# Optimization experiments

Hardware: AMD Instinct MI355X
Metric: run time of the kernel (lower is better)

The kernel has to match this reference:

```python
import jax, jax.numpy as jnp
import numpy as np

N_NODES = 50000
N_EDGES = 600000
D = 128
ITERATIONS = 3


def setup_inputs() -> dict:
    key = jax.random.key(0)
    k0, k1, k2, k3 = jax.random.split(key, 4)
    node_feats = jax.random.normal(k0, (N_NODES, D), dtype=jnp.float32)
    adjacency = jax.random.randint(k1, (N_EDGES, 2), 0, N_NODES, dtype=jnp.int64)
    scale = 1.0 / np.sqrt(D).astype(np.float32)
    W_emb = jax.random.normal(k2, (D, D), dtype=jnp.float32) * scale
    b_emb = jnp.zeros((D,), dtype=jnp.float32)
    W_upd = jax.random.normal(k3, (D, D), dtype=jnp.float32) * scale
    b_upd = jnp.zeros((D,), dtype=jnp.float32)
    return {
        "node_feats": node_feats,
        "W_emb": W_emb,
        "b_emb": b_emb,
        "W_upd": W_upd,
        "b_upd": b_upd,
        "adjacency": adjacency,
    }


def reference(node_feats, W_emb, b_emb, W_upd, b_upd, adjacency):
    # Embedding layer: Dense + ReLU per node (inference path skips BatchNorm)
    h = jax.nn.relu(node_feats @ W_emb + b_emb)  # [N, D]

    src = adjacency[:, 0]
    dst = adjacency[:, 1]

    # Each undirected edge contributes a message in both directions.
    ones = jnp.ones((N_EDGES,), dtype=h.dtype)
    deg = (jax.ops.segment_sum(ones, src, num_segments=N_NODES)
           + jax.ops.segment_sum(ones, dst, num_segments=N_NODES))  # [N]
    denom = (deg + 1.0)[:, None]  # +1 for the node's own contribution

    for _ in range(ITERATIONS):
        # MessagePassing: gather neighbor features, scatter-add into nodes,
        # then normalize by (num incoming messages + 1).
        agg = (jax.ops.segment_sum(h[dst], src, num_segments=N_NODES)
               + jax.ops.segment_sum(h[src], dst, num_segments=N_NODES))  # [N, D]
        h = (h + agg) / denom
        # Update: per-node Dense followed by sigmoid nonlinearity.
        h = jax.nn.sigmoid(h @ W_upd + b_upd)
    return h
```

## Files before the change

kernel.cpp:

```cpp
#include <hip/hip_runtime.h>
#include <hip/hip_bf16.h>

#define NN 50000
#define NE 600000
#define DD 128
#define RB 64
#define NSHARD_DIV 6250
#define GB ((NN + RB - 1) / RB)
#define EBQ ((NE + 1023) / 1024)
#define SB ((NN + 1023) / 1024)
#define GQB3 (2 * ((NN + 31) / 32))

typedef __bf16 bfrag __attribute__((ext_vector_type(8)));
typedef float  ffrag __attribute__((ext_vector_type(4)));
typedef unsigned uintv4 __attribute__((ext_vector_type(4)));
typedef unsigned uintv2 __attribute__((ext_vector_type(2)));

union frag_cast { uintv4 u4; unsigned u[4]; bfrag b; };

__device__ __forceinline__ float bfbits2f(unsigned v) { return __uint_as_float(v << 16); }
__device__ __forceinline__ unsigned f2bfbits(float f) {
    unsigned u = __float_as_uint(f);
    return (u + 0x7FFFu + ((u >> 16) & 1u)) >> 16;
}

__device__ __forceinline__ float ld_in(const void* p, int idx, int f32) {
    return f32 ? ((const float*)p)[idx]
               : bfbits2f(((const unsigned short*)p)[idx]);
}

__device__ __forceinline__ void ld_edge_nt(const int* adj, int e, int i64, int& s, int& d) {
    if (i64) {
        s = __builtin_nontemporal_load(&adj[4 * e]);
        d = __builtin_nontemporal_load(&adj[4 * e + 2]);
    } else {
        s = __builtin_nontemporal_load(&adj[2 * e]);
        d = __builtin_nontemporal_load(&adj[2 * e + 1]);
    }
}

__global__ void k_prep(const unsigned* __restrict__ Ww, const unsigned* __restrict__ adjw,
                       const void* __restrict__ We, const void* __restrict__ Wu,
                       unsigned short* __restrict__ WeT, unsigned short* __restrict__ WuT,
                       int* __restrict__ flags, int* __restrict__ deg) {
    const int tid = threadIdx.x;
    if (blockIdx.x < DD) {
        __shared__ int scnt;
        if (tid == 0) scnt = 0;
        __syncthreads();
        int c = 0;
        for (int i = tid; i < 512; i += 256) {
            unsigned e = (Ww[i] >> 7) & 0xFFu;
            c += (e >= 0x60u && e <= 0x85u) ? 1 : 0;
        }
        atomicAdd(&scnt, c);
        __syncthreads();
        const int f32 = (scnt >= 256) ? 0 : 1;
        const int k = blockIdx.x;
        if (tid < DD) {
            WeT[tid * DD + k] = (unsigned short)f2bfbits(ld_in(We, k * DD + tid, f32));
        } else {
            int n = tid - DD;
            WuT[n * DD + k] = (unsigned short)f2bfbits(ld_in(Wu, k * DD + n, f32));
        }
        return;
    }
    for (int i = (blockIdx.x - DD) * 256 + tid; i < NN; i += 64 * 256) deg[i] = 0;
    if (blockIdx.x != DD) return;
    __shared__ int cnt[2];
    if (tid < 2) cnt[tid] = 0;
    __syncthreads();
    int c0 = 0, c1 = 0;
    for (int i = tid; i < 512; i += 256) {
        unsigned e = (Ww[i] >> 7) & 0xFFu;
        c0 += (e >= 0x60u && e <= 0x85u) ? 1 : 0;
        c1 += (adjw[2 * i + 1] == 0u) ? 1 : 0;
    }
    atomicAdd(&cnt[0], c0);
    atomicAdd(&cnt[1], c1);
    __syncthreads();
    if (tid == 0) {
        flags[0] = (cnt[0] >= 256) ? 0 : 1;
        flags[1] = (cnt[1] >= 256) ? 1 : 0;
    }
}

__device__ __forceinline__ void stage_w(const uintv4* __restrict__ WTg, uintv4* sW, int tid) {
#pragma unroll
    for (int k = 0; k < 8; k++) {
        int d = k * 256 + tid;
        int m = d & 15, rest = d >> 4;
        int quad = rest & 3, ks = (rest >> 2) & 3, ct = rest >> 4;
        sW[d] = WTg[(ct * 16 + m) * 16 + (ks * 4 + quad)];
    }
}

__device__ __forceinline__ void mfma_rows(const bfrag af[4], const bfrag* sW,
                                          int m, int quad, ffrag acc[8]) {
#pragma unroll
    for (int ks = 0; ks < 4; ks++) {
#pragma unroll
        for (int ct = 0; ct < 8; ct++) {
            bfrag bf_ = sW[((ct * 4 + ks) * 4 + quad) * 16 + m];
            acc[ct] = __builtin_amdgcn_mfma_f32_16x16x32_bf16(af[ks], bf_, acc[ct], 0, 0, 0);
        }
    }
}

__device__ __forceinline__ void st_h2(unsigned short* __restrict__ Hout,
                                      int ct, int m, int orow, float z) {
    Hout[(size_t)(ct >> 2) * (NN * 64) + (size_t)orow * 64 + (ct & 3) * 16 + m] =
        (unsigned short)f2bfbits(z);
}

__launch_bounds__(256, 5)
__global__ void k_main1(const void* __restrict__ Xp, const unsigned short* __restrict__ WTg,
                        const void* __restrict__ Bp, unsigned short* __restrict__ Hout,
                        const int* __restrict__ flags, const int* __restrict__ adj,
                        int* __restrict__ deg, uintv2* __restrict__ edg) {
    __shared__ __align__(16) unsigned short sWT[DD * DD];
    const int tid = threadIdx.x;
    if (blockIdx.x >= GB) {
        const int bb = blockIdx.x - GB;
        const int i64 = flags[1];
#pragma unroll
        for (int k = 0; k < 4; k++) {
            const int e = bb * 1024 + k * 256 + tid;
            if (e < NE) {
                int s, d;
                ld_edge_nt(adj, e, i64, s, d);
                uintv2 out;
                if ((unsigned)s < NN && (unsigned)d < NN) {
                    int ks = atomicAdd(&deg[s], 1);
                    int kd = atomicAdd(&deg[d], 1);
                    out[0] = (unsigned)s | ((unsigned)d << 16);
                    out[1] = (unsigned)ks | ((unsigned)kd << 16);
                } else {
                    out[0] = 0xFFFFFFFFu;
                    out[1] = 0;
                }
                __builtin_nontemporal_store(out, &edg[e]);
            }
        }
        return;
    }
    const int wave = tid >> 6;
    const int lane = tid & 63;
    const int f32  = flags[0];
    const int m    = lane & 15;
    const int quad = lane >> 4;
    const int rowbase = blockIdx.x * RB + wave * 16;
    const int row  = rowbase + m;
    const int rc   = (row < NN) ? row : (NN - 1);

    stage_w((const uintv4*)WTg, (uintv4*)sWT, tid);

    bfrag af[4];
    if (f32) {
        const float4* Xf = (const float4*)Xp;
#pragma unroll
        for (int ks = 0; ks < 4; ks++) {
            const int k0 = ks * 32 + quad * 8;
            float4 a0 = Xf[rc * 32 + (k0 >> 2)];
            float4 a1 = Xf[rc * 32 + (k0 >> 2) + 1];
            frag_cast fc;
            fc.u[0] = f2bfbits(a0.x) | (f2bfbits(a0.y) << 16);
            fc.u[1] = f2bfbits(a0.z) | (f2bfbits(a0.w) << 16);
            fc.u[2] = f2bfbits(a1.x) | (f2bfbits(a1.y) << 16);
            fc.u[3] = f2bfbits(a1.z) | (f2bfbits(a1.w) << 16);
            af[ks] = fc.b;
        }
    } else {
        const uintv4* Xv = (const uintv4*)Xp;
#pragma unroll
        for (int ks = 0; ks < 4; ks++) {
            const int k0 = ks * 32 + quad * 8;
            frag_cast fc;
            fc.u4 = Xv[rc * 16 + (k0 >> 3)];
            af[ks] = fc.b;
        }
    }
    __syncthreads();

    ffrag acc[8];
#pragma unroll
    for (int i = 0; i < 8; i++) acc[i] = (ffrag)(0.0f);
    mfma_rows(af, (const bfrag*)sWT, m, quad, acc);

#pragma unroll
    for (int ct = 0; ct < 8; ct++) {
        int col = ct * 16 + m;
        float bb = ld_in(Bp, col, f32);
#pragma unroll
        for (int reg = 0; reg < 4; reg++) {
            int orow = rowbase + quad * 4 + reg;
            if (orow < NN) {
                float z = fmaxf(acc[ct][reg] + bb, 0.0f);
                st_h2(Hout, ct, m, orow, z);
            }
        }
    }
}

__global__ void k_scan1(const int* __restrict__ deg, int* __restrict__ rows,
                        int* __restrict__ sums, int* __restrict__ bhist) {
    __shared__ int wsum[16];
    __shared__ int woff[16];
    __shared__ int hist[256];
    const int tid  = threadIdx.x;
    const int wid  = tid >> 6;
    const int lane = tid & 63;
    const int i = blockIdx.x * 1024 + tid;
    if (tid < 256) hist[tid] = 0;
    __syncthreads();
    int x = (i < NN) ? deg[i] : 0;
    if (i < NN) atomicAdd(&hist[(x < 255) ? x : 255], 1);
#pragma unroll
    for (int off = 1; off < 64; off <<= 1) {
        int y = __shfl_up(x, off, 64);
        if (lane >= off) x += y;
    }
    if (lane == 63) wsum[wid] = x;
    __syncthreads();
    if (wid == 0) {
        int s  = (lane < 16) ? wsum[lane] : 0;
        int xs = s;
#pragma unroll
        for (int off = 1; off < 16; off <<= 1) {
            int y = __shfl_up(xs, off, 64);
            if (lane >= off) xs += y;
        }
        if (lane < 16) woff[lane] = xs - s;
        if (lane == 15) sums[blockIdx.x] = xs;
    }
    __syncthreads();
    if (i < NN) rows[i + 1] = x + woff[wid];
    if (tid < 256) bhist[blockIdx.x * 256 + tid] = hist[tid];
}

__global__ void k_scan2(int* __restrict__ sums, int nb,
                        const int* __restrict__ bhist, int* __restrict__ boff,
                        int* __restrict__ bbase) {
    __shared__ int wps[4];
    const int t = threadIdx.x, lane = t & 63, w = t >> 6;
    if (w == 0) {
        int v = (lane < nb) ? sums[lane] : 0;
        int x = v;
        for (int off = 1; off < 64; off <<= 1) {
            int y = __shfl_up(x, off, 64);
            if (lane >= off) x += y;
        }
        if (lane < nb) sums[lane] = x - v;
    }
    int run = 0;
    for (int blk = 0; blk < nb; blk++) {
        int c = bhist[blk * 256 + t];
        boff[blk * 256 + t] = run;
        run += c;
    }
    int v = run, x = v;
    for (int off = 1; off < 64; off <<= 1) {
        int y = __shfl_up(x, off, 64);
        if (lane >= off) x += y;
    }
    if (lane == 63) wps[w] = x;
    __syncthreads();
    int add = 0;
    for (int k = 0; k < w; k++) add += wps[k];
    bbase[t] = x - v + add;
}

__global__ void k_scan3(const int* __restrict__ sums, int* __restrict__ rows,
                        const int* __restrict__ deg, const int* __restrict__ boff,
                        const int* __restrict__ bbase, int* __restrict__ order) {
    __shared__ int lh[256];
    const int tid = threadIdx.x;
    if (tid < 256) lh[tid] = 0;
    __syncthreads();
    int i = blockIdx.x * 1024 + tid;
    int d = 0, r = 0;
    if (i < NN) {
        rows[i + 1] += sums[blockIdx.x];
        if (i == 0) rows[0] = 0;
        d = deg[i];
        d = (d < 255) ? d : 255;
        r = atomicAdd(&lh[d], 1);
        order[bbase[d] + boff[blockIdx.x * 256 + d] + r] = i;
    }
}

__launch_bounds__(256)
__global__ void k_fill2(const uintv2* __restrict__ edg, const int* __restrict__ rows,
                        unsigned short* __restrict__ nbr) {
    const int shard = blockIdx.x & 7;
    const int bb = blockIdx.x >> 3;
#pragma unroll
    for (int k = 0; k < 4; k++) {
        const int e = bb * 1024 + k * 256 + threadIdx.x;
        if (e >= NE) continue;
        uintv2 v = __builtin_nontemporal_load(&edg[e]);
        if (v[0] == 0xFFFFFFFFu) continue;
        const int s = v[0] & 0xFFFFu, d = v[0] >> 16;
        if (s / NSHARD_DIV == shard) nbr[rows[s] + (v[1] & 0xFFFFu)] = (unsigned short)d;
        if (d / NSHARD_DIV == shard) nbr[rows[d] + (v[1] >> 16)]    = (unsigned short)s;
    }
}

__device__ __forceinline__ void accv4(float a[8], uintv4 v) {
#pragma unroll
    for (int k = 0; k < 4; k++) {
        a[2 * k]     += bfbits2f(v[k] & 0xFFFFu);
        a[2 * k + 1] += bfbits2f(v[k] >> 16);
    }
}

__launch_bounds__(256)
__global__ void k_gath5(const unsigned* __restrict__ Hp, const int* __restrict__ rows,
                        const unsigned short* __restrict__ nbr,
                        const int* __restrict__ order, unsigned* __restrict__ XB32) {
    const int plane = blockIdx.x & 1;
    const int chunk = blockIdx.x >> 1;
    const int g     = threadIdx.x >> 3;
    const int l8    = threadIdx.x & 7;
    const int opos  = chunk * 32 + g;
    const int nid   = order[(opos < NN) ? opos : (NN - 1)];
    const uintv4* Pv = (const uintv4*)Hp + (size_t)plane * (NN * 8);
    const int st = rows[nid], en = rows[nid + 1];
    uintv4 sv = Pv[(size_t)nid * 8 + l8];
    float a[8];
#pragma unroll
    for (int k = 0; k < 4; k++) {
        a[2 * k]     = bfbits2f(sv[k] & 0xFFFFu);
        a[2 * k + 1] = bfbits2f(sv[k] >> 16);
    }
    int j = st;
    for (; j + 8 <= en; j += 8) {
        int n[8];
#pragma unroll
        for (int t = 0; t < 8; t++) n[t] = nbr[j + t];
        uintv4 v[8];
#pragma unroll
        for (int t = 0; t < 8; t++) v[t] = Pv[(size_t)n[t] * 8 + l8];
#pragma unroll
        for (int t = 0; t < 8; t++) accv4(a, v[t]);
    }
    for (; j < en; ++j) accv4(a, Pv[(size_t)nbr[j] * 8 + l8]);
    const float inv = 1.0f / (float)(en - st + 1);
    if (opos < NN) {
        uintv4 pk;
#pragma unroll
        for (int k = 0; k < 4; k++)
            pk[k] = f2bfbits(a[2 * k] * inv) | (f2bfbits(a[2 * k + 1] * inv) << 16);
        __builtin_nontemporal_store(pk, (uintv4*)XB32 + (size_t)nid * 16 + plane * 8 + l8);
    }
}

__launch_bounds__(256, 5)
__global__ void k_gemmB(const unsigned short* __restrict__ XB,
                        const unsigned short* __restrict__ WTg, const void* __restrict__ Bp,
                        unsigned short* __restrict__ HoutBf, float* __restrict__ HoutF,
                        const int* __restrict__ flags, int last) {
    __shared__ __align__(16) unsigned short sWT[DD * DD];
    const int tid  = threadIdx.x;
    const int wave = tid >> 6;
    const int lane = tid & 63;
    const int f32  = flags[0];
    const int m    = lane & 15;
    const int quad = lane >> 4;
    const int rowbase = blockIdx.x * RB + wave * 16;
    const int row  = rowbase + m;

    stage_w((const uintv4*)WTg, (uintv4*)sWT, tid);

    bfrag af[4];
    const uintv4* Xv = (const uintv4*)XB;
#pragma unroll
    for (int ks = 0; ks < 4; ks++) {
        const int k0 = ks * 32 + quad * 8;
        frag_cast fc;
        fc.u4 = __builtin_nontemporal_load(&Xv[row * 16 + (k0 >> 3)]);
        af[ks] = fc.b;
    }
    __syncthreads();

    ffrag acc[8];
#pragma unroll
    for (int i = 0; i < 8; i++) acc[i] = (ffrag)(0.0f);
    mfma_rows(af, (const bfrag*)sWT, m, quad, acc);

#pragma unroll
    for (int ct = 0; ct < 8; ct++) {
        int col = ct * 16 + m;
        float bb = ld_in(Bp, col, f32);
#pragma unroll
        for (int reg = 0; reg < 4; reg++) {
            int orow = rowbase + quad * 4 + reg;
            if (orow < NN) {
                float s = 1.0f / (1.0f + __expf(-(acc[ct][reg] + bb)));
                if (!last) {
                    st_h2(HoutBf, ct, m, orow, s);
                } else if (f32) {
                    HoutF[orow * DD + col] = s;
                } else {
                    ((unsigned short*)HoutF)[orow * DD + col] = (unsigned short)f2bfbits(s);
                }
            }
        }
    }
}

extern "C" void kernel_launch(void* const* d_in, const int* in_sizes, int n_in,
                              void* d_out, int out_size, void* d_ws, size_t ws_size,
                              hipStream_t stream) {
    const void* X  = d_in[0];
    const void* We = d_in[1];
    const void* be = d_in[2];
    const void* Wu = d_in[3];
    const void* bu = d_in[4];
    const int* adj = (const int*)d_in[5];

    char* p = (char*)d_ws;
    int* FLAGS = (int*)p;                       p += 256;
    int* ROWS  = (int*)p;                       p += ((NN + 1) * 4 + 252) / 256 * 256;
    int* SUMS  = (int*)p;                       p += 256;
    int* BHIST = (int*)p;                       p += ((SB * 256 * 4 + 255) / 256) * 256;
    int* BOFF  = (int*)p;                       p += ((SB * 256 * 4 + 255) / 256) * 256;
    int* BBASE = (int*)p;                       p += 1024;
    int* ORDER = (int*)p;                       p += ((NN * 4 + 255) / 256) * 256;
    unsigned short* NBR = (unsigned short*)p;   p += (size_t)2 * NE * 2;
    unsigned short* WeT = (unsigned short*)p;   p += DD * DD * 2;
    unsigned short* WuT = (unsigned short*)p;   p += DD * DD * 2;
    unsigned short* HW  = (unsigned short*)p;
    uintv2* EDG2 = (uintv2*)p;
    int* DEG = (int*)(p + (size_t)NE * 8);

    unsigned short* HA = (unsigned short*)d_out + (size_t)NN * DD;

    k_prep<<<DD + 64, 256, 0, stream>>>((const unsigned*)We, (const unsigned*)adj,
                                        We, Wu, WeT, WuT, FLAGS, DEG);
    k_main1<<<GB + EBQ, 256, 0, stream>>>(X, WeT, be, HA, FLAGS, adj, DEG, EDG2);
    k_scan1<<<SB, 1024, 0, stream>>>(DEG, ROWS, SUMS, BHIST);
    k_scan2<<<1, 256, 0, stream>>>(SUMS, SB, BHIST, BOFF, BBASE);
    k_scan3<<<SB, 1024, 0, stream>>>(SUMS, ROWS, DEG, BOFF, BBASE, ORDER);
    k_fill2<<<8 * EBQ, 256, 0, stream>>>(EDG2, ROWS, NBR);

    for (int it = 0; it < 3; ++it) {
        int last = (it == 2);
        k_gath5<<<GQB3, 256, 0, stream>>>((const unsigned*)HA, ROWS, NBR, ORDER, (unsigned*)HW);
        k_gemmB<<<GB, 256, 0, stream>>>(HW, WuT, bu, HA, (float*)d_out, FLAGS, last);
    }
}
```

Baseline: 352.2 us.

## Build CSR via two-pass bucket radix sort instead of global atomics

Replaces the global-atomic degree counting and sharded scatter fill with a two-level bucketed radix sort of edge endpoints. It does a per-block shared-memory histogram by node>>8, scans the histogram, scatters packed records into buckets, and then does per-bucket local degree counting and neighbor fill with shared atomics. This targets the contended global atomics and random global scatter of the previous CSR build. In exchange it adds three extra kernel launches and an extra pass over the adjacency, and neighbor order within a row may differ.

```diff
diff --git a/kernel.cpp b/kernel.cpp
--- a/kernel.cpp
+++ b/kernel.cpp
@@ -5,9 +5,9 @@
 #define NE 600000
 #define DD 128
 #define RB 64
-#define NSHARD_DIV 6250
 #define GB ((NN + RB - 1) / RB)
-#define EBQ ((NE + 1023) / 1024)
+#define NBE ((NE + 4095) / 4096)
+#define NBUCK 196
 #define SB ((NN + 1023) / 1024)
 #define GQB3 (2 * ((NN + 31) / 32))
 
@@ -42,7 +42,7 @@
 __global__ void k_prep(const unsigned* __restrict__ Ww, const unsigned* __restrict__ adjw,
                        const void* __restrict__ We, const void* __restrict__ Wu,
                        unsigned short* __restrict__ WeT, unsigned short* __restrict__ WuT,
-                       int* __restrict__ flags, int* __restrict__ deg) {
+                       int* __restrict__ flags) {
     const int tid = threadIdx.x;
     if (blockIdx.x < DD) {
         __shared__ int scnt;
@@ -65,8 +65,6 @@
         }
         return;
     }
-    for (int i = (blockIdx.x - DD) * 256 + tid; i < NN; i += 64 * 256) deg[i] = 0;
-    if (blockIdx.x != DD) return;
     __shared__ int cnt[2];
     if (tid < 2) cnt[tid] = 0;
     __syncthreads();
@@ -117,31 +115,29 @@
 __global__ void k_main1(const void* __restrict__ Xp, const unsigned short* __restrict__ WTg,
                         const void* __restrict__ Bp, unsigned short* __restrict__ Hout,
                         const int* __restrict__ flags, const int* __restrict__ adj,
-                        int* __restrict__ deg, uintv2* __restrict__ edg) {
+                        int* __restrict__ bh1) {
     __shared__ __align__(16) unsigned short sWT[DD * DD];
     const int tid = threadIdx.x;
     if (blockIdx.x >= GB) {
+        int* hist = (int*)sWT;
         const int bb = blockIdx.x - GB;
+        hist[tid] = 0;
+        __syncthreads();
         const int i64 = flags[1];
 #pragma unroll
-        for (int k = 0; k < 4; k++) {
-            const int e = bb * 1024 + k * 256 + tid;
+        for (int k = 0; k < 16; k++) {
+            const int e = bb * 4096 + k * 256 + tid;
             if (e < NE) {
                 int s, d;
                 ld_edge_nt(adj, e, i64, s, d);
-                uintv2 out;
                 if ((unsigned)s < NN && (unsigned)d < NN) {
-                    int ks = atomicAdd(&deg[s], 1);
-                    int kd = atomicAdd(&deg[d], 1);
-                    out[0] = (unsigned)s | ((unsigned)d << 16);
-                    out[1] = (unsigned)ks | ((unsigned)kd << 16);
-                } else {
-                    out[0] = 0xFFFFFFFFu;
-                    out[1] = 0;
+                    atomicAdd(&hist[s >> 8], 1);
+                    atomicAdd(&hist[d >> 8], 1);
                 }
-                __builtin_nontemporal_store(out, &edg[e]);
             }
         }
+        __syncthreads();
+        if (tid < NBUCK) bh1[tid * NBE + bb] = hist[tid];
         return;
     }
     const int wave = tid >> 6;
@@ -200,6 +196,96 @@
             }
         }
     }
+}
+
+__global__ void k_scanB(const int* __restrict__ bh1, int* __restrict__ bkoff,
+                        int* __restrict__ bkbase) {
+    __shared__ int tot[256];
+    __shared__ int wps[4];
+    const int t = threadIdx.x, lane = t & 63, w = t >> 6;
+    for (int k = w; k < NBUCK; k += 16) {
+        int vals[3];
+#pragma unroll
+        for (int c = 0; c < 3; c++) {
+            int idx = c * 64 + lane;
+            vals[c] = (idx < NBE) ? bh1[k * NBE + idx] : 0;
+        }
+        int carry = 0;
+#pragma unroll
+        for (int c = 0; c < 3; c++) {
+            int v = vals[c], x = v;
+#pragma unroll
+            for (int off = 1; off < 64; off <<= 1) {
+                int y = __shfl_up(x, off, 64);
+                if (lane >= off) x += y;
+            }
+            int idx = c * 64 + lane;
+            if (idx < NBE) bkoff[k * NBE + idx] = carry + x - v;
+            carry += __shfl(x, 63, 64);
+        }
+        if (lane == 0) tot[k] = carry;
+    }
+    if (t < 256 && t >= NBUCK) tot[t] = 0;
+    __syncthreads();
+    int v = 0, x = 0;
+    if (t < 256) {
+        v = tot[t]; x = v;
+#pragma unroll
+        for (int off = 1; off < 64; off <<= 1) {
+            int y = __shfl_up(x, off, 64);
+            if (lane >= off) x += y;
+        }
+        if (lane == 63) wps[w] = x;
+    }
+    __syncthreads();
+    if (t < NBUCK) {
+        int add = 0;
+        for (int k = 0; k < w; k++) add += wps[k];
+        bkbase[t] = x - v + add;
+        if (t == NBUCK - 1) bkbase[NBUCK] = x + add;
+    }
+}
+
+__launch_bounds__(256)
+__global__ void k_p1b(const int* __restrict__ adj, const int* __restrict__ flags,
+                      const int* __restrict__ bkbase, const int* __restrict__ bkoff,
+                      unsigned* __restrict__ rec) {
+    __shared__ int cur[256];
+    const int tid = threadIdx.x;
+    const int bb = blockIdx.x;
+    if (tid < NBUCK) cur[tid] = bkbase[tid] + bkoff[tid * NBE + bb];
+    __syncthreads();
+    const int i64 = flags[1];
+#pragma unroll
+    for (int k = 0; k < 16; k++) {
+        const int e = bb * 4096 + k * 256 + tid;
+        if (e < NE) {
+            int s, d;
+            ld_edge_nt(adj, e, i64, s, d);
+            if ((unsigned)s < NN && (unsigned)d < NN) {
+                int ps = atomicAdd(&cur[s >> 8], 1);
+                rec[ps] = (unsigned)s | ((unsigned)d << 16);
+                int pd = atomicAdd(&cur[d >> 8], 1);
+                rec[pd] = (unsigned)d | ((unsigned)s << 16);
+            }
+        }
+    }
+}
+
+__launch_bounds__(256)
+__global__ void k_p2a(const unsigned* __restrict__ rec, const int* __restrict__ bkbase,
+                      int* __restrict__ deg) {
+    __shared__ int dh[256];
+    const int tid = threadIdx.x;
+    const int k = blockIdx.x;
+    dh[tid] = 0;
+    __syncthreads();
+    const int st = bkbase[k], en = bkbase[k + 1];
+    for (int j = st + tid; j < en; j += 256)
+        atomicAdd(&dh[rec[j] & 255], 1);
+    __syncthreads();
+    const int node = k * 256 + tid;
+    if (node < NN) deg[node] = dh[tid];
 }
 
 __global__ void k_scan1(const int* __restrict__ deg, int* __restrict__ rows,
@@ -290,19 +376,19 @@
 }
 
 __launch_bounds__(256)
-__global__ void k_fill2(const uintv2* __restrict__ edg, const int* __restrict__ rows,
-                        unsigned short* __restrict__ nbr) {
-    const int shard = blockIdx.x & 7;
-    const int bb = blockIdx.x >> 3;
-#pragma unroll
-    for (int k = 0; k < 4; k++) {
-        const int e = bb * 1024 + k * 256 + threadIdx.x;
-        if (e >= NE) continue;
-        uintv2 v = __builtin_nontemporal_load(&edg[e]);
-        if (v[0] == 0xFFFFFFFFu) continue;
-        const int s = v[0] & 0xFFFFu, d = v[0] >> 16;
-        if (s / NSHARD_DIV == shard) nbr[rows[s] + (v[1] & 0xFFFFu)] = (unsigned short)d;
-        if (d / NSHARD_DIV == shard) nbr[rows[d] + (v[1] >> 16)]    = (unsigned short)s;
+__global__ void k_p2b(const unsigned* __restrict__ rec, const int* __restrict__ bkbase,
+                      const int* __restrict__ rows, unsigned short* __restrict__ nbr) {
+    __shared__ int lcur[256];
+    const int tid = threadIdx.x;
+    const int k = blockIdx.x;
+    const int node = k * 256 + tid;
+    lcur[tid] = (node < NN) ? rows[node] : 0;
+    __syncthreads();
+    const int st = bkbase[k], en = bkbase[k + 1];
+    for (int j = st + tid; j < en; j += 256) {
+        unsigned r = rec[j];
+        int slot = atomicAdd(&lcur[r & 255], 1);
+        nbr[slot] = (unsigned short)(r >> 16);
     }
 }
 
@@ -427,22 +513,28 @@
     int* BOFF  = (int*)p;                       p += ((SB * 256 * 4 + 255) / 256) * 256;
     int* BBASE = (int*)p;                       p += 1024;
     int* ORDER = (int*)p;                       p += ((NN * 4 + 255) / 256) * 256;
+    int* DEG   = (int*)p;                       p += ((NN * 4 + 255) / 256) * 256;
     unsigned short* NBR = (unsigned short*)p;   p += (size_t)2 * NE * 2;
     unsigned short* WeT = (unsigned short*)p;   p += DD * DD * 2;
     unsigned short* WuT = (unsigned short*)p;   p += DD * DD * 2;
+    int* BH1   = (int*)p;                       p += ((NBUCK * NBE * 4 + 255) / 256) * 256;
+    int* BKOFF = (int*)p;                       p += ((NBUCK * NBE * 4 + 255) / 256) * 256;
+    int* BKBASE = (int*)p;                      p += 1024;
     unsigned short* HW  = (unsigned short*)p;
-    uintv2* EDG2 = (uintv2*)p;
-    int* DEG = (int*)(p + (size_t)NE * 8);
+    unsigned* REC = (unsigned*)p;
 
     unsigned short* HA = (unsigned short*)d_out + (size_t)NN * DD;
 
-    k_prep<<<DD + 64, 256, 0, stream>>>((const unsigned*)We, (const unsigned*)adj,
-                                        We, Wu, WeT, WuT, FLAGS, DEG);
-    k_main1<<<GB + EBQ, 256, 0, stream>>>(X, WeT, be, HA, FLAGS, adj, DEG, EDG2);
+    k_prep<<<DD + 1, 256, 0, stream>>>((const unsigned*)We, (const unsigned*)adj,
+                                       We, Wu, WeT, WuT, FLAGS);
+    k_main1<<<GB + NBE, 256, 0, stream>>>(X, WeT, be, HA, FLAGS, adj, BH1);
+    k_scanB<<<1, 1024, 0, stream>>>(BH1, BKOFF, BKBASE);
+    k_p1b<<<NBE, 256, 0, stream>>>(adj, FLAGS, BKBASE, BKOFF, REC);
+    k_p2a<<<NBUCK, 256, 0, stream>>>(REC, BKBASE, DEG);
     k_scan1<<<SB, 1024, 0, stream>>>(DEG, ROWS, SUMS, BHIST);
     k_scan2<<<1, 256, 0, stream>>>(SUMS, SB, BHIST, BOFF, BBASE);
     k_scan3<<<SB, 1024, 0, stream>>>(SUMS, ROWS, DEG, BOFF, BBASE, ORDER);
-    k_fill2<<<8 * EBQ, 256, 0, stream>>>(EDG2, ROWS, NBR);
+    k_p2b<<<NBUCK, 256, 0, stream>>>(REC, BKBASE, ROWS, NBR);
 
     for (int it = 0; it < 3; ++it) {
         int last = (it == 2);
```

Result: faster. 327.6 us (-7.0%).
